# Kernel tuning notes

Hardware: AMD Instinct MI355X
Metric: run time of the kernel (lower is better)

## Reference

```python
import jax, jax.numpy as jnp
import numpy as np

LAMDA = 1.0


def setup_inputs() -> dict:
    key = jax.random.key(0)
    k1, k2, k3, k4 = jax.random.split(key, 4)
    B, C, D = 16384, 1000, 512
    logits = jax.random.normal(k1, (B, C), dtype=jnp.float32)
    labels = jax.random.randint(k2, (B,), 0, C, dtype=jnp.int64)
    features = jax.random.normal(k3, (B, D), dtype=jnp.float32)
    global_protos = jax.random.normal(k4, (C, D), dtype=jnp.float32)
    return {"logits": logits, "labels": labels, "features": features,
            "global_protos": global_protos}


def reference(logits, labels, features, global_protos):
    # --- classification loss: mean cross-entropy ---
    logp = jax.nn.log_softmax(logits, axis=-1)                 # [B, C]
    ce_loss = -jnp.take_along_axis(logp, labels[:, None], axis=1).mean()
    ce_loss = jnp.where(jnp.isfinite(ce_loss), ce_loss, 0.0)

    # --- prototype alignment loss ---
    # Every label has a (finite) global prototype, so the per-sample dict
    # loop reduces to: gather proto by label, per-sample MSE, mean over B.
    gathered = global_protos[labels]                           # [B, D]
    per_sample_mse = jnp.mean((features - gathered) ** 2, axis=-1)  # [B]
    proto_loss = per_sample_mse.mean()

    total_loss = ce_loss + LAMDA * proto_loss
    total_loss = jnp.where(jnp.isfinite(total_loss), total_loss, ce_loss)
    return (total_loss, ce_loss, proto_loss)
```

## Files before the change

kernel.cpp:

```cpp
#include <hip/hip_runtime.h>
#include <math.h>


#ifndef INFINITY
#define INFINITY __builtin_inff()
#endif

__device__ __forceinline__ float safe_exp(float dm) {
    return __expf(fminf(dm, 0.0f));
}

__global__ __launch_bounds__(256) void fedtgp_rows(
    const float* __restrict__ logits,
    const int*   __restrict__ labels,
    const float* __restrict__ features,
    const float* __restrict__ protos,
    double* __restrict__ ce_part,
    double* __restrict__ pl_part,
    int B, int C, int D)
{
    const int tid  = threadIdx.x;
    const int lane = tid & 63;
    const int wv   = tid >> 6;
    const int row  = blockIdx.x * 4 + wv;

    __shared__ double sc[4], sp[4];

    float ce_b = 0.f, pl_b = 0.f;
    bool valid = (row < B);

    if (valid) {
        const int   lab  = labels[row];
        const float* lrow = logits + (size_t)row * C;
        const int C4 = C >> 2;
        const int D4 = D >> 2;

        float m = -INFINITY;
        float s = 0.f;
        float q = 0.f;

        for (int base = 0; base < C4; base += 256) {
            const float4* l4 = (const float4*)lrow;
            float4 v[4];
            #pragma unroll
            for (int k = 0; k < 4; ++k) {
                const int idx = base + lane + 64 * k;
                v[k] = (idx < C4) ? l4[idx]
                                  : make_float4(-INFINITY, -INFINITY, -INFINITY, -INFINITY);
            }
            float cm = m;
            #pragma unroll
            for (int k = 0; k < 4; ++k)
                cm = fmaxf(cm, fmaxf(fmaxf(v[k].x, v[k].y), fmaxf(v[k].z, v[k].w)));
            s *= safe_exp(m - cm);
            #pragma unroll
            for (int k = 0; k < 4; ++k) {
                s += safe_exp(v[k].x - cm) + safe_exp(v[k].y - cm)
                   + safe_exp(v[k].z - cm) + safe_exp(v[k].w - cm);
            }
            m = cm;
        }
        for (int c = (C4 << 2) + lane; c < C; c += 64) {
            const float x  = lrow[c];
            const float cm = fmaxf(m, x);
            s = s * safe_exp(m - cm) + safe_exp(x - cm);
            m = cm;
        }

        {
            const float4* f4 = (const float4*)(features + (size_t)row * D);
            const float4* p4 = (const float4*)(protos   + (size_t)lab * D);
            #pragma unroll
            for (int k = 0; k < 2; ++k) {
                const int idx = lane + 64 * k;
                float4 f = make_float4(0.f, 0.f, 0.f, 0.f);
                float4 p = make_float4(0.f, 0.f, 0.f, 0.f);
                if (idx < D4) { f = f4[idx]; p = p4[idx]; }
                const float dx = f.x - p.x, dy = f.y - p.y;
                const float dz = f.z - p.z, dw = f.w - p.w;
                q += dx * dx + dy * dy + dz * dz + dw * dw;
            }
            for (int idx = lane + 128; idx < D4; idx += 64) {
                const float4 f = f4[idx];
                const float4 p = p4[idx];
                const float dx = f.x - p.x, dy = f.y - p.y;
                const float dz = f.z - p.z, dw = f.w - p.w;
                q += dx * dx + dy * dy + dz * dz + dw * dw;
            }
            for (int d = (D4 << 2) + lane; d < D; d += 64) {
                const float df = features[(size_t)row * D + d]
                               - protos[(size_t)lab * D + d];
                q += df * df;
            }
        }

        #pragma unroll
        for (int off = 32; off > 0; off >>= 1) {
            const float om = __shfl_xor(m, off, 64);
            const float os = __shfl_xor(s, off, 64);
            q += __shfl_xor(q, off, 64);
            const float nm = fmaxf(m, om);
            s = s * safe_exp(m - nm) + os * safe_exp(om - nm);
            m = nm;
        }

        const float ll  = lrow[lab];
        const float lse = m + __logf(s);
        ce_b = lse - ll;
        pl_b = q / (float)D;
    }

    if (lane == 0) {
        sc[wv] = valid ? (double)ce_b : 0.0;
        sp[wv] = valid ? (double)pl_b : 0.0;
    }
    __syncthreads();
    if (tid == 0) {
        ce_part[blockIdx.x] = sc[0] + sc[1] + sc[2] + sc[3];
        pl_part[blockIdx.x] = sp[0] + sp[1] + sp[2] + sp[3];
    }
}

__global__ __launch_bounds__(1024) void fedtgp_finalize(
    const double* __restrict__ ce_part,
    const double* __restrict__ pl_part,
    float* __restrict__ out,
    int npart, double invB)
{
    const int tid  = threadIdx.x;
    const int lane = tid & 63;
    const int wv   = tid >> 6;
    __shared__ double rc[16];
    __shared__ double rp[16];

    double c = 0.0, p = 0.0;
    for (int i = tid; i < npart; i += 1024) {
        c += ce_part[i];
        p += pl_part[i];
    }
    #pragma unroll
    for (int off = 32; off > 0; off >>= 1) {
        c += __shfl_xor(c, off, 64);
        p += __shfl_xor(p, off, 64);
    }
    if (lane == 0) { rc[wv] = c; rp[wv] = p; }
    __syncthreads();

    if (tid == 0) {
        double cs = 0.0, ps = 0.0;
        #pragma unroll
        for (int k = 0; k < 16; ++k) { cs += rc[k]; ps += rp[k]; }
        float ce = (float)(cs * invB);
        float pl = (float)(ps * invB);
        if (!isfinite(ce)) ce = 0.0f;
        float tot = ce + pl;
        if (!isfinite(tot)) tot = ce;
        out[0] = tot;
        out[1] = ce;
        out[2] = pl;
    }
}

extern "C" void kernel_launch(void* const* d_in, const int* in_sizes, int n_in,
                              void* d_out, int out_size, void* d_ws, size_t ws_size,
                              hipStream_t stream)
{
    const float* logits   = (const float*)d_in[0];
    const int*   labels   = (const int*)  d_in[1];
    const float* features = (const float*)d_in[2];
    const float* protos   = (const float*)d_in[3];
    float* out = (float*)d_out;

    const int B = in_sizes[1];
    const int C = in_sizes[0] / B;
    const int D = in_sizes[2] / B;

    int nb = (B + 3) / 4;
    const size_t need_per_block = 2 * sizeof(double);
    if ((size_t)nb * need_per_block > ws_size) {
        nb = (int)(ws_size / need_per_block);
        if (nb < 1) nb = 1;
    }

    double* ce_part = (double*)d_ws;
    double* pl_part = ce_part + nb;

    fedtgp_rows<<<nb, 256, 0, stream>>>(logits, labels, features, protos,
                                        ce_part, pl_part, B, C, D);
    fedtgp_finalize<<<1, 1024, 0, stream>>>(ce_part, pl_part, out, nb,
                                            1.0 / (double)B);
}
```

Measured before the change: 121.1 us.

## Fuse finalize into row kernel via atomics and hoist all loads early

```diff
diff --git a/kernel.cpp b/kernel.cpp
--- a/kernel.cpp
+++ b/kernel.cpp
@@ -6,18 +6,25 @@
 #define INFINITY __builtin_inff()
 #endif
 
+struct Accum {
+    double ce;
+    double pl;
+    unsigned int cnt;
+    unsigned int pad[3];
+};
+
 __device__ __forceinline__ float safe_exp(float dm) {
     return __expf(fminf(dm, 0.0f));
 }
 
-__global__ __launch_bounds__(256) void fedtgp_rows(
+__global__ __launch_bounds__(256) void fedtgp_fused(
     const float* __restrict__ logits,
     const int*   __restrict__ labels,
     const float* __restrict__ features,
     const float* __restrict__ protos,
-    double* __restrict__ ce_part,
-    double* __restrict__ pl_part,
-    int B, int C, int D)
+    Accum* __restrict__ acc,
+    float* __restrict__ out,
+    int B, int C, int D, double invB)
 {
     const int tid  = threadIdx.x;
     const int lane = tid & 63;
@@ -27,27 +34,32 @@
     __shared__ double sc[4], sp[4];
 
     float ce_b = 0.f, pl_b = 0.f;
-    bool valid = (row < B);
+    const bool valid = (row < B);
 
     if (valid) {
-        const int   lab  = labels[row];
+        const int    lab  = labels[row];
         const float* lrow = logits + (size_t)row * C;
+        const float4* l4  = (const float4*)lrow;
         const int C4 = C >> 2;
         const int D4 = D >> 2;
 
-        float m = -INFINITY;
-        float s = 0.f;
-        float q = 0.f;
+        float4 v[4];
+        #pragma unroll
+        for (int k = 0; k < 4; ++k) {
+            const int idx = lane + 64 * k;
+            v[k] = (idx < C4) ? l4[idx]
+                              : make_float4(-INFINITY, -INFINITY, -INFINITY, -INFINITY);
+        }
+        const float4* f4 = (const float4*)(features + (size_t)row * D);
+        const float4* p4 = (const float4*)(protos   + (size_t)lab * D);
+        float4 f0 = make_float4(0.f,0.f,0.f,0.f), p0 = f0;
+        float4 f1 = f0, p1 = f0;
+        if (lane < D4)      { f0 = f4[lane];      p0 = p4[lane]; }
+        if (lane + 64 < D4) { f1 = f4[lane + 64]; p1 = p4[lane + 64]; }
+        const float ll = lrow[lab];
 
-        for (int base = 0; base < C4; base += 256) {
-            const float4* l4 = (const float4*)lrow;
-            float4 v[4];
-            #pragma unroll
-            for (int k = 0; k < 4; ++k) {
-                const int idx = base + lane + 64 * k;
-                v[k] = (idx < C4) ? l4[idx]
-                                  : make_float4(-INFINITY, -INFINITY, -INFINITY, -INFINITY);
-            }
+        float m = -INFINITY, s = 0.f;
+        {
             float cm = m;
             #pragma unroll
             for (int k = 0; k < 4; ++k)
@@ -60,6 +72,19 @@
             }
             m = cm;
         }
+        for (int base = 256; base < C4; base += 256) {
+            #pragma unroll
+            for (int k = 0; k < 4; ++k) {
+                const int idx = base + lane + 64 * k;
+                const float4 w = (idx < C4) ? l4[idx]
+                    : make_float4(-INFINITY, -INFINITY, -INFINITY, -INFINITY);
+                const float cm = fmaxf(m, fmaxf(fmaxf(w.x, w.y), fmaxf(w.z, w.w)));
+                s = s * safe_exp(m - cm)
+                  + safe_exp(w.x - cm) + safe_exp(w.y - cm)
+                  + safe_exp(w.z - cm) + safe_exp(w.w - cm);
+                m = cm;
+            }
+        }
         for (int c = (C4 << 2) + lane; c < C; c += 64) {
             const float x  = lrow[c];
             const float cm = fmaxf(m, x);
@@ -67,31 +92,26 @@
             m = cm;
         }
 
+        float q;
         {
-            const float4* f4 = (const float4*)(features + (size_t)row * D);
-            const float4* p4 = (const float4*)(protos   + (size_t)lab * D);
-            #pragma unroll
-            for (int k = 0; k < 2; ++k) {
-                const int idx = lane + 64 * k;
-                float4 f = make_float4(0.f, 0.f, 0.f, 0.f);
-                float4 p = make_float4(0.f, 0.f, 0.f, 0.f);
-                if (idx < D4) { f = f4[idx]; p = p4[idx]; }
-                const float dx = f.x - p.x, dy = f.y - p.y;
-                const float dz = f.z - p.z, dw = f.w - p.w;
-                q += dx * dx + dy * dy + dz * dz + dw * dw;
-            }
-            for (int idx = lane + 128; idx < D4; idx += 64) {
-                const float4 f = f4[idx];
-                const float4 p = p4[idx];
-                const float dx = f.x - p.x, dy = f.y - p.y;
-                const float dz = f.z - p.z, dw = f.w - p.w;
-                q += dx * dx + dy * dy + dz * dz + dw * dw;
-            }
-            for (int d = (D4 << 2) + lane; d < D; d += 64) {
-                const float df = features[(size_t)row * D + d]
-                               - protos[(size_t)lab * D + d];
-                q += df * df;
-            }
+            const float ax = f0.x - p0.x, ay = f0.y - p0.y;
+            const float az = f0.z - p0.z, aw = f0.w - p0.w;
+            const float bx = f1.x - p1.x, by = f1.y - p1.y;
+            const float bz = f1.z - p1.z, bw = f1.w - p1.w;
+            q = ax*ax + ay*ay + az*az + aw*aw
+              + bx*bx + by*by + bz*bz + bw*bw;
+        }
+        for (int idx = lane + 128; idx < D4; idx += 64) {
+            const float4 f = f4[idx];
+            const float4 p = p4[idx];
+            const float dx = f.x - p.x, dy = f.y - p.y;
+            const float dz = f.z - p.z, dw = f.w - p.w;
+            q += dx*dx + dy*dy + dz*dz + dw*dw;
+        }
+        for (int d = (D4 << 2) + lane; d < D; d += 64) {
+            const float df = features[(size_t)row * D + d]
+                           - protos[(size_t)lab * D + d];
+            q += df * df;
         }
 
         #pragma unroll
@@ -104,7 +124,6 @@
             m = nm;
         }
 
-        const float ll  = lrow[lab];
         const float lse = m + __logf(s);
         ce_b = lse - ll;
         pl_b = q / (float)D;
@@ -115,49 +134,24 @@
         sp[wv] = valid ? (double)pl_b : 0.0;
     }
     __syncthreads();
-    if (tid == 0) {
-        ce_part[blockIdx.x] = sc[0] + sc[1] + sc[2] + sc[3];
-        pl_part[blockIdx.x] = sp[0] + sp[1] + sp[2] + sp[3];
-    }
-}
-
-__global__ __launch_bounds__(1024) void fedtgp_finalize(
-    const double* __restrict__ ce_part,
-    const double* __restrict__ pl_part,
-    float* __restrict__ out,
-    int npart, double invB)
-{
-    const int tid  = threadIdx.x;
-    const int lane = tid & 63;
-    const int wv   = tid >> 6;
-    __shared__ double rc[16];
-    __shared__ double rp[16];
-
-    double c = 0.0, p = 0.0;
-    for (int i = tid; i < npart; i += 1024) {
-        c += ce_part[i];
-        p += pl_part[i];
-    }
-    #pragma unroll
-    for (int off = 32; off > 0; off >>= 1) {
-        c += __shfl_xor(c, off, 64);
-        p += __shfl_xor(p, off, 64);
-    }
-    if (lane == 0) { rc[wv] = c; rp[wv] = p; }
-    __syncthreads();
 
     if (tid == 0) {
-        double cs = 0.0, ps = 0.0;
-        #pragma unroll
-        for (int k = 0; k < 16; ++k) { cs += rc[k]; ps += rp[k]; }
-        float ce = (float)(cs * invB);
-        float pl = (float)(ps * invB);
-        if (!isfinite(ce)) ce = 0.0f;
-        float tot = ce + pl;
-        if (!isfinite(tot)) tot = ce;
-        out[0] = tot;
-        out[1] = ce;
-        out[2] = pl;
+        atomicAdd(&acc->ce, sc[0] + sc[1] + sc[2] + sc[3]);
+        atomicAdd(&acc->pl, sp[0] + sp[1] + sp[2] + sp[3]);
+        __threadfence();
+        const unsigned prev = atomicAdd(&acc->cnt, 1u);
+        if (prev == (unsigned)(gridDim.x - 1)) {
+            const double cs = atomicAdd(&acc->ce, 0.0);
+            const double ps = atomicAdd(&acc->pl, 0.0);
+            float ce = (float)(cs * invB);
+            float pl = (float)(ps * invB);
+            if (!isfinite(ce)) ce = 0.0f;
+            float tot = ce + pl;
+            if (!isfinite(tot)) tot = ce;
+            out[0] = tot;
+            out[1] = ce;
+            out[2] = pl;
+        }
     }
 }
 
@@ -175,18 +169,11 @@
     const int C = in_sizes[0] / B;
     const int D = in_sizes[2] / B;
 
-    int nb = (B + 3) / 4;
-    const size_t need_per_block = 2 * sizeof(double);
-    if ((size_t)nb * need_per_block > ws_size) {
-        nb = (int)(ws_size / need_per_block);
-        if (nb < 1) nb = 1;
-    }
+    const int nb = (B + 3) / 4;
 
-    double* ce_part = (double*)d_ws;
-    double* pl_part = ce_part + nb;
+    Accum* acc = (Accum*)d_ws;
+    hipMemsetAsync(d_ws, 0, sizeof(Accum), stream);
 
-    fedtgp_rows<<<nb, 256, 0, stream>>>(logits, labels, features, protos,
-                                        ce_part, pl_part, B, C, D);
-    fedtgp_finalize<<<1, 1024, 0, stream>>>(ce_part, pl_part, out, nb,
-                                            1.0 / (double)B);
+    fedtgp_fused<<<nb, 256, 0, stream>>>(logits, labels, features, protos,
+                                         acc, out, B, C, D, 1.0 / (double)B);
 }
```

Result: slower. 293.3 us (+142.2%).
